# Optimization experiments

Hardware: AMD Instinct MI355X
Metric: run time of the kernel (lower is better)

## Reference

```python
import jax, jax.numpy as jnp
import numpy as np
import math

XLEN, YLEN, B = 2048, 1024, 8
XD, YD, HD, YOUT = 1024, 1024, 512, 1024


def setup_inputs() -> dict:
    key = jax.random.key(0)
    ks = jax.random.split(key, 12)

    def lin(kw, kb, out_d, in_d):
        s = 1.0 / math.sqrt(in_d)
        w = jax.random.uniform(kw, (out_d, in_d), jnp.float32, -s, s)
        b = jax.random.uniform(kb, (out_d,), jnp.float32, -s, s)
        return w, b

    Xk_w, Xk_b = lin(ks[0], ks[1], HD, XD)
    Xv_w, Xv_b = lin(ks[2], ks[3], HD, XD)
    Yq_w, Yq_b = lin(ks[4], ks[5], HD, YD)
    Yw_w, Yw_b = lin(ks[6], ks[7], YOUT, YD + HD)

    X = jax.random.normal(ks[8], (XLEN, B, XD), jnp.float32)
    Y = jax.random.normal(ks[9], (YLEN, B, YD), jnp.float32)
    alignment = jax.random.normal(ks[10], (B, YLEN, XLEN), jnp.float32)
    X_pad_mask = jax.random.bernoulli(ks[11], 0.1, (B, YLEN, XLEN))  # True -> mask out
    align_w = jnp.zeros((1,), jnp.float32)  # nn.Parameter([0])

    return {"X": X, "Y": Y, "alignment": alignment, "X_pad_mask": X_pad_mask,
            "Xk_w": Xk_w, "Xk_b": Xk_b, "Xv_w": Xv_w, "Xv_b": Xv_b,
            "Yq_w": Yq_w, "Yq_b": Yq_b, "Yw_w": Yw_w, "Yw_b": Yw_b,
            "align_w": align_w}


def reference(X, Y, alignment, X_pad_mask, Xk_w, Xk_b, Xv_w, Xv_b,
              Yq_w, Yq_b, Yw_w, Yw_b, align_w):
    FMAX = jnp.finfo(X.dtype).max
    # projections (torch Linear: x @ W.T + b)
    xk = X @ Xk_w.T + Xk_b                     # (x, b, hd)
    yq = Y @ Yq_w.T + Yq_b                     # (y, b, hd)
    # scaled cross-attention logits
    logit = jnp.einsum('xbd,ybd->byx', xk, yq) / math.sqrt(xk.shape[-1])
    # gated alignment bias + clamp
    logit = logit + jax.nn.sigmoid(align_w[0]) * alignment
    logit = jnp.maximum(logit, -FMAX)
    # pad-mask additive fill (-FMAX) then clamp (matches masked_fill + add + clamp)
    logit = jnp.maximum(logit + jnp.where(X_pad_mask, -FMAX, 0.0), -FMAX)
    attn = jax.nn.softmax(logit, axis=-1)      # (b, y, x); dropout = identity (eval)
    xv = X @ Xv_w.T + Xv_b                     # (x, b, hd)
    attn_feat = jnp.einsum('byx,xbh->ybh', attn, xv)  # (y, b, hd)
    concat = jnp.concatenate([Y, attn_feat], axis=-1)  # (y, b, yd+hd)
    return concat @ Yw_w.T + Yw_b              # (y, b, y_outdim)
```

## Files before the change

kernel.cpp:

```cpp
#include <hip/hip_runtime.h>


#define FMAXF 3.402823466e38f

typedef __attribute__((ext_vector_type(8))) __bf16 bf16x8;
typedef __attribute__((ext_vector_type(4))) float f32x4;

static __device__ __forceinline__ short f2b(float f) {
  union { float f; unsigned u; } x; x.f = f;
  unsigned r = (x.u + 0x7FFFu + ((x.u >> 16) & 1u)) >> 16;
  return (short)r;
}
static __device__ __forceinline__ float b2f(short s) {
  union { unsigned u; float f; } x; x.u = ((unsigned)(unsigned short)s) << 16;
  return x.f;
}

static __device__ __forceinline__ void gl_lds16(const short* g, short* l) {
  __builtin_amdgcn_global_load_lds(
      (const __attribute__((address_space(1))) void*)g,
      (__attribute__((address_space(3))) void*)l, 16, 0, 0);
}


struct EpiKV {
  short* xk; short* xv; const float* kb; const float* vb;
  __device__ void operator()(int bz, int m, int n, float v) const {
    int b = m & 7; long x = m >> 3;
    if (n < 512) {
      xk[((long)b * 2048 + x) * 512 + n] = f2b(v + kb[n]);
    } else {
      xv[((long)b * 2048 + x) * 512 + (n - 512)] = f2b(v + vb[n - 512]);
    }
  }
};

struct EpiYq {
  short* out; const float* bias;
  __device__ void operator()(int bz, int m, int n, float v) const {
    out[(((long)(m & 7)) * 1024 + (m >> 3)) * 512 + n] = f2b(v + bias[n]);
  }
};

struct EpiLogit {
  short* out;
  __device__ void operator()(int bz, int m, int n, float v) const {
    out[((long)bz * 1024 + m) * 2048 + n] = f2b(v);
  }
};

struct EpiConcat {
  short* out;
  __device__ void operator()(int bz, int m, int n, float v) const {
    out[((long)m * 8 + bz) * 1536 + 1024 + n] = f2b(v);
  }
};

struct EpiOut {
  float* out; const float* bias;
  __device__ void operator()(int bz, int m, int n, float v) const {
    out[(long)m * 1024 + n] = v + bias[n];
  }
};

template <int TM, typename Epi>
__global__ __launch_bounds__(256) void gemm_mt(
    const short* __restrict__ A, long sAb, int lda,
    const short* __restrict__ B, long sBb, int ldb,
    int K, int tlog, Epi epi) {
  constexpr int R = TM + 128;
  constexpr int SEGS = R / 64;
  __shared__ short S[R * 32];

  const int tid = threadIdx.x;
  const int lane = tid & 63, wave = tid >> 6;
  const int bz = blockIdx.z;

  const int id = blockIdx.x;
  const int xcd = id & 7;
  const int r = id >> 3;
  const int n0 = (r & ((1 << tlog) - 1)) * 128;
  const int m0 = (((r >> tlog) << 3) + xcd) * TM;

  const short* gp[SEGS];
#pragma unroll
  for (int t = 0; t < SEGS; t++) {
    int seg = t * 256 + tid;
    int row = seg >> 2, col = (seg & 3) * 8;
    gp[t] = (row < TM)
                ? A + (long)bz * sAb + (long)(m0 + row) * lda + col
                : B + (long)bz * sBb + (long)(n0 + row - TM) * ldb + col;
  }

  const int wm = (TM == 128) ? (wave & 1) * 64 : 0;
  const int wn = (TM == 128) ? (wave >> 1) * 64 : wave * 32;
  constexpr int MI = 4;
  constexpr int MJ = (TM == 128) ? 4 : 2;
  const int quad = lane >> 4, l16 = lane & 15;

  f32x4 acc[MI][MJ] = {};

  for (int k0 = 0; k0 < K; k0 += 32) {
#pragma unroll
    for (int t = 0; t < SEGS; t++)
      gl_lds16(gp[t] + k0, S + (t * 256 + tid) * 8);
    __syncthreads();

    union { int4 v; bf16x8 f; } a[MI], b[MJ];
#pragma unroll
    for (int i = 0; i < MI; i++)
      a[i].v = *(const int4*)(S + (wm + i * 16 + l16) * 32 + quad * 8);
#pragma unroll
    for (int j = 0; j < MJ; j++)
      b[j].v = *(const int4*)(S + (TM + wn + j * 16 + l16) * 32 + quad * 8);
#pragma unroll
    for (int i = 0; i < MI; i++)
#pragma unroll
      for (int j = 0; j < MJ; j++)
        acc[i][j] = __builtin_amdgcn_mfma_f32_16x16x32_bf16(a[i].f, b[j].f,
                                                            acc[i][j], 0, 0, 0);
    __syncthreads();
  }

#pragma unroll
  for (int i = 0; i < MI; i++)
#pragma unroll
    for (int j = 0; j < MJ; j++)
#pragma unroll
      for (int r4 = 0; r4 < 4; r4++)
        epi(bz, m0 + wm + i * 16 + quad * 4 + r4, n0 + wn + j * 16 + l16,
            acc[i][j][r4]);
}

__global__ __launch_bounds__(256) void cvt_f32_bf16(const float* __restrict__ in,
                                                    short* __restrict__ out,
                                                    long n4) {
  long i = (long)blockIdx.x * 256 + threadIdx.x;
  if (i >= n4) return;
  float4 f = ((const float4*)in)[i];
  union { short s[4]; long long v; } o;
  o.s[0] = f2b(f.x); o.s[1] = f2b(f.y); o.s[2] = f2b(f.z); o.s[3] = f2b(f.w);
  ((long long*)out)[i] = o.v;
}

__global__ __launch_bounds__(256) void cvt_y_concat(const float* __restrict__ in,
                                                    short* __restrict__ out) {
  long idx = (long)blockIdx.x * 256 + threadIdx.x;
  long row = idx >> 8;
  int c = (int)(idx & 255) << 2;
  float4 f = *(const float4*)(in + row * 1024 + c);
  union { short s[4]; unsigned long long v; } o;
  o.s[0] = f2b(f.x); o.s[1] = f2b(f.y); o.s[2] = f2b(f.z); o.s[3] = f2b(f.w);
  *(unsigned long long*)(out + row * 1536 + c) = o.v;
}

__global__ __launch_bounds__(256) void transpose_xv(const short* __restrict__ xv,
                                                    short* __restrict__ xvt) {
  __shared__ short t[32][36];
  const int b = blockIdx.z;
  const long x0 = (long)blockIdx.x * 32, h0 = (long)blockIdx.y * 32;
  const int r = threadIdx.x >> 3, c = (threadIdx.x & 7) * 4;
  const short* src = xv + ((long)b * 2048 + x0 + r) * 512 + h0 + c;
  *(int2*)&t[r][c] = *(const int2*)src;
  __syncthreads();
  union { short s[4]; int2 v; } o;
  o.s[0] = t[c + 0][r]; o.s[1] = t[c + 1][r];
  o.s[2] = t[c + 2][r]; o.s[3] = t[c + 3][r];
  short* dst = xvt + ((long)b * 512 + h0 + r) * 2048 + x0 + c;
  *(int2*)dst = o.v;
}

__global__ __launch_bounds__(256) void softmax_rows(short* __restrict__ logits,
                                                    const float* __restrict__ align,
                                                    const int* __restrict__ mask,
                                                    const float* __restrict__ alw) {
  const long row = blockIdx.x;
  const long base = row * 2048 + threadIdx.x * 8;
  short* p = logits + base;
  const float g = 1.0f / (1.0f + __expf(-alw[0]));
  const float scale = 0.04419417382415922f;

  union { short s[8]; int4 v; } d;
  d.v = *(const int4*)p;
  float4 al0 = *(const float4*)(align + base);
  float4 al1 = *(const float4*)(align + base + 4);
  int4 mk0 = *(const int4*)(mask + base);
  int4 mk1 = *(const int4*)(mask + base + 4);

  float vals[8];
  vals[0] = mk0.x ? -FMAXF : b2f(d.s[0]) * scale + g * al0.x;
  vals[1] = mk0.y ? -FMAXF : b2f(d.s[1]) * scale + g * al0.y;
  vals[2] = mk0.z ? -FMAXF : b2f(d.s[2]) * scale + g * al0.z;
  vals[3] = mk0.w ? -FMAXF : b2f(d.s[3]) * scale + g * al0.w;
  vals[4] = mk1.x ? -FMAXF : b2f(d.s[4]) * scale + g * al1.x;
  vals[5] = mk1.y ? -FMAXF : b2f(d.s[5]) * scale + g * al1.y;
  vals[6] = mk1.z ? -FMAXF : b2f(d.s[6]) * scale + g * al1.z;
  vals[7] = mk1.w ? -FMAXF : b2f(d.s[7]) * scale + g * al1.w;

  float mx = -FMAXF;
#pragma unroll
  for (int i = 0; i < 8; i++) mx = fmaxf(mx, vals[i]);
#pragma unroll
  for (int off = 32; off; off >>= 1) mx = fmaxf(mx, __shfl_xor(mx, off));
  __shared__ float redm[4], reds[4];
  const int tid = threadIdx.x;
  if ((tid & 63) == 0) redm[tid >> 6] = mx;
  __syncthreads();
  mx = fmaxf(fmaxf(redm[0], redm[1]), fmaxf(redm[2], redm[3]));

  float s = 0.0f;
#pragma unroll
  for (int i = 0; i < 8; i++) { vals[i] = __expf(vals[i] - mx); s += vals[i]; }
#pragma unroll
  for (int off = 32; off; off >>= 1) s += __shfl_xor(s, off);
  if ((tid & 63) == 0) reds[tid >> 6] = s;
  __syncthreads();
  s = reds[0] + reds[1] + reds[2] + reds[3];
  float inv = 1.0f / s;
#pragma unroll
  for (int i = 0; i < 8; i++) d.s[i] = f2b(vals[i] * inv);
  *(int4*)p = d.v;
}


extern "C" void kernel_launch(void* const* d_in, const int* in_sizes, int n_in,
                              void* d_out, int out_size, void* d_ws, size_t ws_size,
                              hipStream_t stream) {
  const float* X    = (const float*)d_in[0];
  const float* Y    = (const float*)d_in[1];
  const float* alig = (const float*)d_in[2];
  const int*   mask = (const int*)d_in[3];
  const float* Xk_w = (const float*)d_in[4];
  const float* Xk_b = (const float*)d_in[5];
  const float* Xv_w = (const float*)d_in[6];
  const float* Xv_b = (const float*)d_in[7];
  const float* Yq_w = (const float*)d_in[8];
  const float* Yq_b = (const float*)d_in[9];
  const float* Yw_w = (const float*)d_in[10];
  const float* Yw_b = (const float*)d_in[11];
  const float* alw  = (const float*)d_in[12];
  float* out = (float*)d_out;

  char* ws = (char*)d_ws;
  short* xbf    = (short*)(ws + 0);
  short* logits = (short*)(ws + 0);
  short* xk     = (short*)(ws + 33554432);
  short* xv     = (short*)(ws + 50331648);
  short* xvt    = (short*)(ws + 67108864);
  short* yq     = (short*)(ws + 83886080);
  short* concat = (short*)(ws + 92274688);
  short* wkv    = (short*)(ws + 117440512);
  short* wyq    = (short*)(ws + 119537664);
  short* wyw    = (short*)(ws + 120586240);

  cvt_f32_bf16<<<16384, 256, 0, stream>>>(X, xbf, 4194304);
  cvt_y_concat<<<8192, 256, 0, stream>>>(Y, concat);
  cvt_f32_bf16<<<512, 256, 0, stream>>>(Xk_w, wkv, 131072);
  cvt_f32_bf16<<<512, 256, 0, stream>>>(Xv_w, wkv + 512 * 1024, 131072);
  cvt_f32_bf16<<<512, 256, 0, stream>>>(Yq_w, wyq, 131072);
  cvt_f32_bf16<<<1536, 256, 0, stream>>>(Yw_w, wyw, 393216);

  gemm_mt<128, EpiKV><<<dim3(1024, 1, 1), 256, 0, stream>>>(
      xbf, 0, 1024, wkv, 0, 1024, 1024, 3, EpiKV{xk, xv, Xk_b, Xv_b});

  gemm_mt<64, EpiYq><<<dim3(512, 1, 1), 256, 0, stream>>>(
      concat, 0, 1536, wyq, 0, 1024, 1024, 2, EpiYq{yq, Yq_b});

  transpose_xv<<<dim3(64, 16, 8), 256, 0, stream>>>(xv, xvt);

  gemm_mt<128, EpiLogit><<<dim3(128, 1, 8), 256, 0, stream>>>(
      yq, (long)1024 * 512, 512, xk, (long)2048 * 512, 512, 512, 4,
      EpiLogit{logits});

  softmax_rows<<<8192, 256, 0, stream>>>(logits, alig, mask, alw);

  gemm_mt<64, EpiConcat><<<dim3(64, 1, 8), 256, 0, stream>>>(
      logits, (long)1024 * 2048, 2048, xvt, (long)512 * 2048, 2048, 2048, 2,
      EpiConcat{concat});

  gemm_mt<128, EpiOut><<<dim3(512, 1, 1), 256, 0, stream>>>(
      concat, 0, 1536, wyw, 0, 1536, 1536, 3, EpiOut{out, Yw_b});
}
```

Measured before the change: 459.4 us.

## Deepen GEMM K-tile, swizzle LDS, stage vectorized epilogue, merge weight conversions

```diff
diff --git a/kernel.cpp b/kernel.cpp
--- a/kernel.cpp
+++ b/kernel.cpp
@@ -24,41 +24,47 @@
 
 
 struct EpiKV {
+  static constexpr bool staged = true;
   short* xk; short* xv; const float* kb; const float* vb;
-  __device__ void operator()(int bz, int m, int n, float v) const {
+  __device__ float bias_at(int n) const { return n < 512 ? kb[n] : vb[n - 512]; }
+  __device__ void store(int bz, int m, int n, int4 v) const {
     int b = m & 7; long x = m >> 3;
-    if (n < 512) {
-      xk[((long)b * 2048 + x) * 512 + n] = f2b(v + kb[n]);
-    } else {
-      xv[((long)b * 2048 + x) * 512 + (n - 512)] = f2b(v + vb[n - 512]);
-    }
+    if (n < 512) *(int4*)(xk + ((long)b * 2048 + x) * 512 + n) = v;
+    else         *(int4*)(xv + ((long)b * 2048 + x) * 512 + (n - 512)) = v;
   }
 };
 
 struct EpiYq {
+  static constexpr bool staged = true;
   short* out; const float* bias;
-  __device__ void operator()(int bz, int m, int n, float v) const {
-    out[(((long)(m & 7)) * 1024 + (m >> 3)) * 512 + n] = f2b(v + bias[n]);
+  __device__ float bias_at(int n) const { return bias[n]; }
+  __device__ void store(int bz, int m, int n, int4 v) const {
+    *(int4*)(out + (((long)(m & 7)) * 1024 + (m >> 3)) * 512 + n) = v;
   }
 };
 
 struct EpiLogit {
+  static constexpr bool staged = true;
   short* out;
-  __device__ void operator()(int bz, int m, int n, float v) const {
-    out[((long)bz * 1024 + m) * 2048 + n] = f2b(v);
+  __device__ float bias_at(int n) const { return 0.0f; }
+  __device__ void store(int bz, int m, int n, int4 v) const {
+    *(int4*)(out + ((long)bz * 1024 + m) * 2048 + n) = v;
   }
 };
 
 struct EpiConcat {
+  static constexpr bool staged = true;
   short* out;
-  __device__ void operator()(int bz, int m, int n, float v) const {
-    out[((long)m * 8 + bz) * 1536 + 1024 + n] = f2b(v);
+  __device__ float bias_at(int n) const { return 0.0f; }
+  __device__ void store(int bz, int m, int n, int4 v) const {
+    *(int4*)(out + ((long)m * 8 + bz) * 1536 + 1024 + n) = v;
   }
 };
 
 struct EpiOut {
+  static constexpr bool staged = false;
   float* out; const float* bias;
-  __device__ void operator()(int bz, int m, int n, float v) const {
+  __device__ void direct(int bz, int m, int n, float v) const {
     out[(long)m * 1024 + n] = v + bias[n];
   }
 };
@@ -69,8 +75,9 @@
     const short* __restrict__ B, long sBb, int ldb,
     int K, int tlog, Epi epi) {
   constexpr int R = TM + 128;
-  constexpr int SEGS = R / 64;
-  __shared__ short S[R * 32];
+  constexpr int SEGS = R / 32;
+  constexpr int LDSN = (R * 64 > TM * 128) ? R * 64 : TM * 128;
+  __shared__ short S[LDSN];
 
   const int tid = threadIdx.x;
   const int lane = tid & 63, wave = tid >> 6;
@@ -78,18 +85,19 @@
 
   const int id = blockIdx.x;
   const int xcd = id & 7;
-  const int r = id >> 3;
-  const int n0 = (r & ((1 << tlog) - 1)) * 128;
-  const int m0 = (((r >> tlog) << 3) + xcd) * TM;
+  const int rr = id >> 3;
+  const int n0 = (rr & ((1 << tlog) - 1)) * 128;
+  const int m0 = (((rr >> tlog) << 3) + xcd) * TM;
 
   const short* gp[SEGS];
 #pragma unroll
   for (int t = 0; t < SEGS; t++) {
-    int seg = t * 256 + tid;
-    int row = seg >> 2, col = (seg & 3) * 8;
+    int slot = t * 256 + tid;
+    int row = slot >> 3;
+    int gcol = ((slot & 7) ^ (row & 7)) * 8;
     gp[t] = (row < TM)
-                ? A + (long)bz * sAb + (long)(m0 + row) * lda + col
-                : B + (long)bz * sBb + (long)(n0 + row - TM) * ldb + col;
+                ? A + (long)bz * sAb + (long)(m0 + row) * lda + gcol
+                : B + (long)bz * sBb + (long)(n0 + row - TM) * ldb + gcol;
   }
 
   const int wm = (TM == 128) ? (wave & 1) * 64 : 0;
@@ -97,39 +105,65 @@
   constexpr int MI = 4;
   constexpr int MJ = (TM == 128) ? 4 : 2;
   const int quad = lane >> 4, l16 = lane & 15;
+  const int xr = l16 & 7;
 
   f32x4 acc[MI][MJ] = {};
 
-  for (int k0 = 0; k0 < K; k0 += 32) {
+  for (int k0 = 0; k0 < K; k0 += 64) {
 #pragma unroll
     for (int t = 0; t < SEGS; t++)
       gl_lds16(gp[t] + k0, S + (t * 256 + tid) * 8);
     __syncthreads();
 
-    union { int4 v; bf16x8 f; } a[MI], b[MJ];
+#pragma unroll
+    for (int kk = 0; kk < 2; kk++) {
+      union { int4 v; bf16x8 f; } a[MI], b[MJ];
+      const int g = ((kk << 2) + quad);
+#pragma unroll
+      for (int i = 0; i < MI; i++)
+        a[i].v = *(const int4*)(S + (wm + i * 16 + l16) * 64 + (g ^ xr) * 8);
+#pragma unroll
+      for (int j = 0; j < MJ; j++)
+        b[j].v = *(const int4*)(S + (TM + wn + j * 16 + l16) * 64 + (g ^ xr) * 8);
+#pragma unroll
+      for (int i = 0; i < MI; i++)
+#pragma unroll
+        for (int j = 0; j < MJ; j++)
+          acc[i][j] = __builtin_amdgcn_mfma_f32_16x16x32_bf16(a[i].f, b[j].f,
+                                                              acc[i][j], 0, 0, 0);
+    }
+    __syncthreads();
+  }
+
+  if constexpr (Epi::staged) {
+#pragma unroll
+    for (int j = 0; j < MJ; j++) {
+      const int c = wn + j * 16 + l16;
+      const float bj = epi.bias_at(n0 + c);
+#pragma unroll
+      for (int i = 0; i < MI; i++)
+#pragma unroll
+        for (int r = 0; r < 4; r++)
+          S[(wm + i * 16 + quad * 4 + r) * 128 + c] = f2b(acc[i][j][r] + bj);
+    }
+    __syncthreads();
+#pragma unroll
+    for (int t = 0; t < TM / 16; t++) {
+      int c = t * 256 + tid;
+      int row = c >> 4, colc = (c & 15) * 8;
+      int4 v = *(const int4*)(S + row * 128 + colc);
+      epi.store(bz, m0 + row, n0 + colc, v);
+    }
+  } else {
 #pragma unroll
     for (int i = 0; i < MI; i++)
-      a[i].v = *(const int4*)(S + (wm + i * 16 + l16) * 32 + quad * 8);
-#pragma unroll
-    for (int j = 0; j < MJ; j++)
-      b[j].v = *(const int4*)(S + (TM + wn + j * 16 + l16) * 32 + quad * 8);
-#pragma unroll
-    for (int i = 0; i < MI; i++)
 #pragma unroll
       for (int j = 0; j < MJ; j++)
-        acc[i][j] = __builtin_amdgcn_mfma_f32_16x16x32_bf16(a[i].f, b[j].f,
-                                                            acc[i][j], 0, 0, 0);
-    __syncthreads();
-  }
-
-#pragma unroll
-  for (int i = 0; i < MI; i++)
-#pragma unroll
-    for (int j = 0; j < MJ; j++)
-#pragma unroll
-      for (int r4 = 0; r4 < 4; r4++)
-        epi(bz, m0 + wm + i * 16 + quad * 4 + r4, n0 + wn + j * 16 + l16,
-            acc[i][j][r4]);
+#pragma unroll
+        for (int r = 0; r < 4; r++)
+          epi.direct(bz, m0 + wm + i * 16 + quad * 4 + r,
+                     n0 + wn + j * 16 + l16, acc[i][j][r]);
+  }
 }
 
 __global__ __launch_bounds__(256) void cvt_f32_bf16(const float* __restrict__ in,
@@ -141,6 +175,22 @@
   union { short s[4]; long long v; } o;
   o.s[0] = f2b(f.x); o.s[1] = f2b(f.y); o.s[2] = f2b(f.z); o.s[3] = f2b(f.w);
   ((long long*)out)[i] = o.v;
+}
+
+__global__ __launch_bounds__(256) void cvt_weights(
+    const float* __restrict__ xk_w, const float* __restrict__ xv_w,
+    const float* __restrict__ yq_w, const float* __restrict__ yw_w,
+    short* __restrict__ wkv, short* __restrict__ wyq, short* __restrict__ wyw) {
+  long i = (long)blockIdx.x * 256 + threadIdx.x;
+  const float* src; long long* dst; long off;
+  if (i < 131072)      { src = xk_w; dst = (long long*)wkv; off = i; }
+  else if (i < 262144) { src = xv_w; dst = (long long*)wkv + 131072; off = i - 131072; }
+  else if (i < 393216) { src = yq_w; dst = (long long*)wyq; off = i - 262144; }
+  else                 { src = yw_w; dst = (long long*)wyw; off = i - 393216; }
+  float4 f = ((const float4*)src)[off];
+  union { short s[4]; long long v; } o;
+  o.s[0] = f2b(f.x); o.s[1] = f2b(f.y); o.s[2] = f2b(f.z); o.s[3] = f2b(f.w);
+  dst[off] = o.v;
 }
 
 __global__ __launch_bounds__(256) void cvt_y_concat(const float* __restrict__ in,
@@ -255,10 +305,7 @@
 
   cvt_f32_bf16<<<16384, 256, 0, stream>>>(X, xbf, 4194304);
   cvt_y_concat<<<8192, 256, 0, stream>>>(Y, concat);
-  cvt_f32_bf16<<<512, 256, 0, stream>>>(Xk_w, wkv, 131072);
-  cvt_f32_bf16<<<512, 256, 0, stream>>>(Xv_w, wkv + 512 * 1024, 131072);
-  cvt_f32_bf16<<<512, 256, 0, stream>>>(Yq_w, wyq, 131072);
-  cvt_f32_bf16<<<1536, 256, 0, stream>>>(Yw_w, wyw, 393216);
+  cvt_weights<<<3072, 256, 0, stream>>>(Xk_w, Xv_w, Yq_w, Yw_w, wkv, wyq, wyw);
 
   gemm_mt<128, EpiKV><<<dim3(1024, 1, 1), 256, 0, stream>>>(
       xbf, 0, 1024, wkv, 0, 1024, 1024, 3, EpiKV{xk, xv, Xk_b, Xv_b});
```

New measurement: 424.7 us. -7.5%, faster.
